# Kernel optimization log

Hardware: AMD Instinct MI355X
Metric: run time of the kernel (lower is better)

The kernel has to match this reference:

```python
import jax, jax.numpy as jnp
import numpy as np

B, SEQ, C_IN, F, K = 32, 16384, 64, 64, 9

def setup_inputs() -> dict:
    key = jax.random.key(0)
    k1, k2 = jax.random.split(key)
    x = jax.random.normal(k1, (B, SEQ, C_IN), dtype=jnp.float32)
    w = jax.random.normal(k2, (F, K, C_IN), dtype=jnp.float32) * 0.05  # mimics random_normal_initializer stddev
    b = jnp.zeros((F,), dtype=jnp.float32)
    return {"x": x, "w": w, "b": b}

def reference(x, w, b):
    # Faithful math: out[bt, t, f] = sum_{k,c} w[f,k,c] * x[bt, t+k, c] + b[f]
    # (VALID padding, stride 1). Expressed as an efficient conv instead of the
    # original unrolled loop + giant stacked intermediate.
    kernel = jnp.transpose(w, (1, 2, 0))  # [K, C_in, F] for WIO layout
    out = jax.lax.conv_general_dilated(
        x, kernel,
        window_strides=(1,),
        padding='VALID',
        dimension_numbers=('NWC', 'WIO', 'NWC'),
    )  # [B, SEQ-K+1, F]
    return out + b[None, None, :]
```

## Files before the change

### kernel.cpp

```cpp
#include <hip/hip_runtime.h>
#include <hip/hip_bf16.h>

#define T_IN   16384
#define T_OUT  16376
#define CIN    64
#define NF     64
#define KT     9
#define NB     32
#define TILE   128
#define ROWS   (TILE + KT - 1)
#define LDS_STRIDE 72
#define TILES_PER_BATCH 128
#define NTILES (NB * TILES_PER_BATCH)
#define NBLOCKS 512
#define TILE_ITERS (NTILES / NBLOCKS)

typedef __bf16 bf16x8 __attribute__((ext_vector_type(8)));
typedef unsigned short u16x8 __attribute__((ext_vector_type(8)));
typedef unsigned short u16x4 __attribute__((ext_vector_type(4)));
typedef float f32x16 __attribute__((ext_vector_type(16)));

__device__ __forceinline__ unsigned short f2bf(float f) {
    unsigned u = __builtin_bit_cast(unsigned, f);
    u += 0x7FFFu + ((u >> 16) & 1u);
    return (unsigned short)(u >> 16);
}

__global__ __launch_bounds__(256, 2) void conv1d_mfma_kernel(
    const float* __restrict__ x,
    const float* __restrict__ w,
    const float* __restrict__ b,
    float* __restrict__ out)
{
    __shared__ __attribute__((aligned(16))) unsigned short ldsX[ROWS * LDS_STRIDE];

    const int tid  = threadIdx.x;
    const int lane = tid & 63;
    const int wv   = tid >> 6;
    const int half = lane >> 5;
    const int l31  = lane & 31;
    const int fh   = wv & 1;
    const int rh   = wv >> 1;
    const int fbase = fh * 32;
    const int rbase = rh * 64;
    const int fcol  = fbase + l31;

    bf16x8 Bf[KT][4];
#pragma unroll
    for (int k = 0; k < KT; ++k) {
#pragma unroll
        for (int s = 0; s < 4; ++s) {
            const float* wp = w + (size_t)fcol * (KT * CIN) + k * CIN + s * 16 + half * 8;
            const float4 w0 = *(const float4*)(wp);
            const float4 w1 = *(const float4*)(wp + 4);
            u16x8 t;
            t[0] = f2bf(w0.x); t[1] = f2bf(w0.y); t[2] = f2bf(w0.z); t[3] = f2bf(w0.w);
            t[4] = f2bf(w1.x); t[5] = f2bf(w1.y); t[6] = f2bf(w1.z); t[7] = f2bf(w1.w);
            Bf[k][s] = __builtin_bit_cast(bf16x8, t);
        }
    }
    const float bias = b[fcol];

    for (int it = 0; it < TILE_ITERS; ++it) {
        const int g  = blockIdx.x * TILE_ITERS + it;
        const int bb = g >> 7;
        const int t0 = (g & 127) << 7;

        for (int i = tid; i < ROWS * 16; i += 256) {
            const int r  = i >> 4;
            const int cg = i & 15;
            int gr = t0 + r;
            gr = gr < (T_IN - 1) ? gr : (T_IN - 1);
            const float4 v = *(const float4*)(x + ((size_t)bb * T_IN + gr) * CIN + cg * 4);
            u16x4 p;
            p[0] = f2bf(v.x); p[1] = f2bf(v.y); p[2] = f2bf(v.z); p[3] = f2bf(v.w);
            *(u16x4*)&ldsX[r * LDS_STRIDE + cg * 4] = p;
        }
        __syncthreads();

        f32x16 acc0 = {0,0,0,0,0,0,0,0,0,0,0,0,0,0,0,0};
        f32x16 acc1 = {0,0,0,0,0,0,0,0,0,0,0,0,0,0,0,0};
        const int abase = (rbase + l31) * LDS_STRIDE + half * 8;
#pragma unroll
        for (int k = 0; k < KT; ++k) {
#pragma unroll
            for (int s = 0; s < 4; ++s) {
                const int off = abase + k * LDS_STRIDE + s * 16;
                bf16x8 a0 = *(const bf16x8*)&ldsX[off];
                bf16x8 a1 = *(const bf16x8*)&ldsX[off + 32 * LDS_STRIDE];
                acc0 = __builtin_amdgcn_mfma_f32_32x32x16_bf16(a0, Bf[k][s], acc0, 0, 0, 0);
                acc1 = __builtin_amdgcn_mfma_f32_32x32x16_bf16(a1, Bf[k][s], acc1, 0, 0, 0);
            }
        }

#pragma unroll
        for (int m = 0; m < 2; ++m) {
            const f32x16 A = m ? acc1 : acc0;
#pragma unroll
            for (int r = 0; r < 16; ++r) {
                const int tl = rbase + m * 32 + (r & 3) + 8 * (r >> 2) + 4 * half;
                const int tg = t0 + tl;
                if (tg < T_OUT)
                    out[((size_t)bb * T_OUT + tg) * NF + fcol] = A[r] + bias;
            }
        }
        __syncthreads();
    }
}

extern "C" void kernel_launch(void* const* d_in, const int* in_sizes, int n_in,
                              void* d_out, int out_size, void* d_ws, size_t ws_size,
                              hipStream_t stream) {
    const float* x = (const float*)d_in[0];
    const float* w = (const float*)d_in[1];
    const float* b = (const float*)d_in[2];
    float* out = (float*)d_out;
    conv1d_mfma_kernel<<<NBLOCKS, 256, 0, stream>>>(x, w, b, out);
}
```

Before: 295.0 us.

## Double-buffer LDS input tiles with register prefetch of next tile

Adds a second LDS buffer and prefetches the next tile's input into registers (9 float4 per thread) before the MFMA loop. After compute it converts the prefetched data to bf16, writes it to the other buffer, and synchronizes once per iteration instead of twice. The aim is to hide global load latency behind MFMA work. In exchange, register pressure rises by 36 VGPRs on top of the 144 already used for the weight fragments, which under launch_bounds(256,2) may cause spills. LDS use also doubles.

```diff
diff --git a/kernel.cpp b/kernel.cpp
--- a/kernel.cpp
+++ b/kernel.cpp
@@ -14,6 +14,8 @@
 #define NTILES (NB * TILES_PER_BATCH)
 #define NBLOCKS 512
 #define TILE_ITERS (NTILES / NBLOCKS)
+#define CHUNKS (ROWS * 16)
+#define CPT 9
 
 typedef __bf16 bf16x8 __attribute__((ext_vector_type(8)));
 typedef unsigned short u16x8 __attribute__((ext_vector_type(8)));
@@ -32,7 +34,7 @@
     const float* __restrict__ b,
     float* __restrict__ out)
 {
-    __shared__ __attribute__((aligned(16))) unsigned short ldsX[ROWS * LDS_STRIDE];
+    __shared__ __attribute__((aligned(16))) unsigned short ldsX[2][ROWS * LDS_STRIDE];
 
     const int tid  = threadIdx.x;
     const int lane = tid & 63;
@@ -61,36 +63,92 @@
     }
     const float bias = b[fcol];
 
-    for (int it = 0; it < TILE_ITERS; ++it) {
-        const int g  = blockIdx.x * TILE_ITERS + it;
+    float4 st[CPT];
+
+    {
+        const int g  = blockIdx.x * TILE_ITERS;
         const int bb = g >> 7;
         const int t0 = (g & 127) << 7;
+#pragma unroll
+        for (int i = 0; i < CPT; ++i) {
+            const int idx = i * 256 + tid;
+            if (idx < CHUNKS) {
+                const int r  = idx >> 4;
+                const int cg = idx & 15;
+                int gr = t0 + r;
+                gr = gr < (T_IN - 1) ? gr : (T_IN - 1);
+                st[i] = *(const float4*)(x + ((size_t)bb * T_IN + gr) * CIN + cg * 4);
+            }
+        }
+#pragma unroll
+        for (int i = 0; i < CPT; ++i) {
+            const int idx = i * 256 + tid;
+            if (idx < CHUNKS) {
+                const int r  = idx >> 4;
+                const int cg = idx & 15;
+                u16x4 p;
+                p[0] = f2bf(st[i].x); p[1] = f2bf(st[i].y);
+                p[2] = f2bf(st[i].z); p[3] = f2bf(st[i].w);
+                *(u16x4*)&ldsX[0][r * LDS_STRIDE + cg * 4] = p;
+            }
+        }
+    }
+    __syncthreads();
 
-        for (int i = tid; i < ROWS * 16; i += 256) {
-            const int r  = i >> 4;
-            const int cg = i & 15;
-            int gr = t0 + r;
-            gr = gr < (T_IN - 1) ? gr : (T_IN - 1);
-            const float4 v = *(const float4*)(x + ((size_t)bb * T_IN + gr) * CIN + cg * 4);
-            u16x4 p;
-            p[0] = f2bf(v.x); p[1] = f2bf(v.y); p[2] = f2bf(v.z); p[3] = f2bf(v.w);
-            *(u16x4*)&ldsX[r * LDS_STRIDE + cg * 4] = p;
+    for (int it = 0; it < TILE_ITERS; ++it) {
+        const int g   = blockIdx.x * TILE_ITERS + it;
+        const int bb  = g >> 7;
+        const int t0  = (g & 127) << 7;
+        const int cur = it & 1;
+        const bool more = (it + 1 < TILE_ITERS);
+
+        if (more) {
+            const int gn  = g + 1;
+            const int bbn = gn >> 7;
+            const int t0n = (gn & 127) << 7;
+#pragma unroll
+            for (int i = 0; i < CPT; ++i) {
+                const int idx = i * 256 + tid;
+                if (idx < CHUNKS) {
+                    const int r  = idx >> 4;
+                    const int cg = idx & 15;
+                    int gr = t0n + r;
+                    gr = gr < (T_IN - 1) ? gr : (T_IN - 1);
+                    st[i] = *(const float4*)(x + ((size_t)bbn * T_IN + gr) * CIN + cg * 4);
+                }
+            }
         }
-        __syncthreads();
 
         f32x16 acc0 = {0,0,0,0,0,0,0,0,0,0,0,0,0,0,0,0};
         f32x16 acc1 = {0,0,0,0,0,0,0,0,0,0,0,0,0,0,0,0};
+        const unsigned short* lx = ldsX[cur];
         const int abase = (rbase + l31) * LDS_STRIDE + half * 8;
 #pragma unroll
         for (int k = 0; k < KT; ++k) {
 #pragma unroll
             for (int s = 0; s < 4; ++s) {
                 const int off = abase + k * LDS_STRIDE + s * 16;
-                bf16x8 a0 = *(const bf16x8*)&ldsX[off];
-                bf16x8 a1 = *(const bf16x8*)&ldsX[off + 32 * LDS_STRIDE];
+                bf16x8 a0 = *(const bf16x8*)&lx[off];
+                bf16x8 a1 = *(const bf16x8*)&lx[off + 32 * LDS_STRIDE];
                 acc0 = __builtin_amdgcn_mfma_f32_32x32x16_bf16(a0, Bf[k][s], acc0, 0, 0, 0);
                 acc1 = __builtin_amdgcn_mfma_f32_32x32x16_bf16(a1, Bf[k][s], acc1, 0, 0, 0);
             }
+        }
+
+        if (more) {
+#pragma unroll
+            for (int i = 0; i < CPT; ++i) {
+                const int idx = i * 256 + tid;
+                if (idx < CHUNKS) {
+                    const int r  = idx >> 4;
+                    const int cg = idx & 15;
+                    u16x4 p;
+                    p[0] = f2bf(st[i].x); p[1] = f2bf(st[i].y);
+                    p[2] = f2bf(st[i].z); p[3] = f2bf(st[i].w);
+                    *(u16x4*)&ldsX[cur ^ 1][r * LDS_STRIDE + cg * 4] = p;
+                }
+            }
+            __syncthreads();
         }
 
 #pragma unroll
@@ -104,7 +162,6 @@
                     out[((size_t)bb * T_OUT + tg) * NF + fcol] = A[r] + bias;
             }
         }
-        __syncthreads();
     }
 }
 
```

After: 303.9 us. +3.0%, slower.

## Prefetch next input tile into LDS via async global_load_lds while computing

Applied to the files above, without the earlier changes.

Introduces an fp32 LDS staging buffer filled through global_load_lds DMA for the next tile while MFMAs run on the current one, then converts it to bf16 in LDS between barriers. This is meant to hide global-load latency behind compute. It adds about 35KB of LDS per block, which may limit occupancy below 2 blocks per CU, and it adds an extra LDS read-convert pass. The output stores now happen after the convert step.

```diff
diff --git a/kernel.cpp b/kernel.cpp
--- a/kernel.cpp
+++ b/kernel.cpp
@@ -14,6 +14,8 @@
 #define NTILES (NB * TILES_PER_BATCH)
 #define NBLOCKS 512
 #define TILE_ITERS (NTILES / NBLOCKS)
+#define CHUNKS (ROWS * 16)
+#define DMA_INSTR (ROWS / 4)
 
 typedef __bf16 bf16x8 __attribute__((ext_vector_type(8)));
 typedef unsigned short u16x8 __attribute__((ext_vector_type(8)));
@@ -26,12 +28,19 @@
     return (unsigned short)(u >> 16);
 }
 
+__device__ __forceinline__ void async_load16(const float* g, float* l) {
+    __builtin_amdgcn_global_load_lds(
+        (const __attribute__((address_space(1))) void*)g,
+        (__attribute__((address_space(3))) void*)l, 16, 0, 0);
+}
+
 __global__ __launch_bounds__(256, 2) void conv1d_mfma_kernel(
     const float* __restrict__ x,
     const float* __restrict__ w,
     const float* __restrict__ b,
     float* __restrict__ out)
 {
+    __shared__ __attribute__((aligned(16))) float          f32X[ROWS * CIN];
     __shared__ __attribute__((aligned(16))) unsigned short ldsX[ROWS * LDS_STRIDE];
 
     const int tid  = threadIdx.x;
@@ -44,6 +53,9 @@
     const int fbase = fh * 32;
     const int rbase = rh * 64;
     const int fcol  = fbase + l31;
+
+    const int dma_r = lane >> 4;
+    const int dma_c = (lane & 15) << 2;
 
     bf16x8 Bf[KT][4];
 #pragma unroll
@@ -61,22 +73,40 @@
     }
     const float bias = b[fcol];
 
-    for (int it = 0; it < TILE_ITERS; ++it) {
-        const int g  = blockIdx.x * TILE_ITERS + it;
+    auto stage = [&](int g) {
         const int bb = g >> 7;
         const int t0 = (g & 127) << 7;
+        for (int j = wv; j < DMA_INSTR; j += 4) {
+            int gr = t0 + j * 4 + dma_r;
+            gr = gr < (T_IN - 1) ? gr : (T_IN - 1);
+            const float* gp = x + ((size_t)bb * T_IN + gr) * CIN + dma_c;
+            async_load16(gp, &f32X[j * 256]);
+        }
+    };
 
-        for (int i = tid; i < ROWS * 16; i += 256) {
+    auto convert = [&]() {
+        for (int i = tid; i < CHUNKS; i += 256) {
+            const float4 v = *(const float4*)&f32X[i * 4];
             const int r  = i >> 4;
             const int cg = i & 15;
-            int gr = t0 + r;
-            gr = gr < (T_IN - 1) ? gr : (T_IN - 1);
-            const float4 v = *(const float4*)(x + ((size_t)bb * T_IN + gr) * CIN + cg * 4);
             u16x4 p;
             p[0] = f2bf(v.x); p[1] = f2bf(v.y); p[2] = f2bf(v.z); p[3] = f2bf(v.w);
             *(u16x4*)&ldsX[r * LDS_STRIDE + cg * 4] = p;
         }
-        __syncthreads();
+    };
+
+    stage(blockIdx.x * TILE_ITERS);
+    __syncthreads();
+    convert();
+    __syncthreads();
+
+    for (int it = 0; it < TILE_ITERS; ++it) {
+        const int g   = blockIdx.x * TILE_ITERS + it;
+        const int bb  = g >> 7;
+        const int t0  = (g & 127) << 7;
+        const bool more = (it + 1 < TILE_ITERS);
+
+        if (more) stage(g + 1);
 
         f32x16 acc0 = {0,0,0,0,0,0,0,0,0,0,0,0,0,0,0,0};
         f32x16 acc1 = {0,0,0,0,0,0,0,0,0,0,0,0,0,0,0,0};
@@ -93,6 +123,10 @@
             }
         }
 
+        __syncthreads();
+        if (more) convert();
+        __syncthreads();
+
 #pragma unroll
         for (int m = 0; m < 2; ++m) {
             const f32x16 A = m ? acc1 : acc0;
@@ -104,7 +138,6 @@
                     out[((size_t)bb * T_OUT + tg) * NF + fcol] = A[r] + bias;
             }
         }
-        __syncthreads();
     }
 }
 
```

Measured after the change: 291.1 us. Within noise of the previous version (-1.3%).

## Double-buffer LDS input tiles and prefetch two tiles ahead in registers

Applied to the files above, without the earlier changes.

Input staging becomes a software pipeline. The next tile's fp32 data is held in registers and converted into a second LDS buffer while the MFMA loop runs. Global loads for the tile two steps ahead are issued inside the k loop. This is meant to hide global load latency and drop one barrier per tile, in exchange for doubled LDS use and nine extra float4 registers per thread, which could reduce occupancy.

```diff
diff --git a/kernel.cpp b/kernel.cpp
--- a/kernel.cpp
+++ b/kernel.cpp
@@ -10,10 +10,9 @@
 #define TILE   128
 #define ROWS   (TILE + KT - 1)
 #define LDS_STRIDE 72
-#define TILES_PER_BATCH 128
-#define NTILES (NB * TILES_PER_BATCH)
 #define NBLOCKS 512
-#define TILE_ITERS (NTILES / NBLOCKS)
+#define TILE_ITERS 8
+#define CHUNKS (ROWS * 16)
 
 typedef __bf16 bf16x8 __attribute__((ext_vector_type(8)));
 typedef unsigned short u16x8 __attribute__((ext_vector_type(8)));
@@ -32,7 +31,7 @@
     const float* __restrict__ b,
     float* __restrict__ out)
 {
-    __shared__ __attribute__((aligned(16))) unsigned short ldsX[ROWS * LDS_STRIDE];
+    __shared__ __attribute__((aligned(16))) unsigned short ldsX[2][ROWS * LDS_STRIDE];
 
     const int tid  = threadIdx.x;
     const int lane = tid & 63;
@@ -41,9 +40,8 @@
     const int l31  = lane & 31;
     const int fh   = wv & 1;
     const int rh   = wv >> 1;
-    const int fbase = fh * 32;
     const int rbase = rh * 64;
-    const int fcol  = fbase + l31;
+    const int fcol  = fh * 32 + l31;
 
     bf16x8 Bf[KT][4];
 #pragma unroll
@@ -61,22 +59,48 @@
     }
     const float bias = b[fcol];
 
+    const int base = blockIdx.x * TILE_ITERS;
+
+    auto load_chunk = [&](int g, int k) -> float4 {
+        const int idx = k * 256 + tid;
+        const int r   = idx >> 4;
+        const int cg  = idx & 15;
+        const int bb2 = g >> 7;
+        int gr = ((g & 127) << 7) + r;
+        gr = gr < (T_IN - 1) ? gr : (T_IN - 1);
+        return *(const float4*)(x + ((size_t)bb2 * T_IN + gr) * CIN + cg * 4);
+    };
+
+    float4 st[KT];
+
+#pragma unroll
+    for (int k = 0; k < KT; ++k)
+        if (k < 8 || tid < 128) st[k] = load_chunk(base, k);
+#pragma unroll
+    for (int k = 0; k < KT; ++k) {
+        if (k < 8 || tid < 128) {
+            const int idx = k * 256 + tid;
+            const int r = idx >> 4, cg = idx & 15;
+            u16x4 p;
+            p[0] = f2bf(st[k].x); p[1] = f2bf(st[k].y);
+            p[2] = f2bf(st[k].z); p[3] = f2bf(st[k].w);
+            *(u16x4*)&ldsX[0][r * LDS_STRIDE + cg * 4] = p;
+        }
+    }
+#pragma unroll
+    for (int k = 0; k < KT; ++k)
+        if (k < 8 || tid < 128) st[k] = load_chunk(base + 1, k);
+    __syncthreads();
+
     for (int it = 0; it < TILE_ITERS; ++it) {
-        const int g  = blockIdx.x * TILE_ITERS + it;
+        const int g  = base + it;
         const int bb = g >> 7;
         const int t0 = (g & 127) << 7;
-
-        for (int i = tid; i < ROWS * 16; i += 256) {
-            const int r  = i >> 4;
-            const int cg = i & 15;
-            int gr = t0 + r;
-            gr = gr < (T_IN - 1) ? gr : (T_IN - 1);
-            const float4 v = *(const float4*)(x + ((size_t)bb * T_IN + gr) * CIN + cg * 4);
-            u16x4 p;
-            p[0] = f2bf(v.x); p[1] = f2bf(v.y); p[2] = f2bf(v.z); p[3] = f2bf(v.w);
-            *(u16x4*)&ldsX[r * LDS_STRIDE + cg * 4] = p;
-        }
-        __syncthreads();
+        const int c  = it & 1;
+        const unsigned short* lx = ldsX[c];
+        unsigned short*       lw = ldsX[c ^ 1];
+        const bool cons = (it < TILE_ITERS - 1);
+        const bool lood = (it < TILE_ITERS - 2);
 
         f32x16 acc0 = {0,0,0,0,0,0,0,0,0,0,0,0,0,0,0,0};
         f32x16 acc1 = {0,0,0,0,0,0,0,0,0,0,0,0,0,0,0,0};
@@ -86,10 +110,21 @@
 #pragma unroll
             for (int s = 0; s < 4; ++s) {
                 const int off = abase + k * LDS_STRIDE + s * 16;
-                bf16x8 a0 = *(const bf16x8*)&ldsX[off];
-                bf16x8 a1 = *(const bf16x8*)&ldsX[off + 32 * LDS_STRIDE];
+                bf16x8 a0 = *(const bf16x8*)&lx[off];
+                bf16x8 a1 = *(const bf16x8*)&lx[off + 32 * LDS_STRIDE];
                 acc0 = __builtin_amdgcn_mfma_f32_32x32x16_bf16(a0, Bf[k][s], acc0, 0, 0, 0);
                 acc1 = __builtin_amdgcn_mfma_f32_32x32x16_bf16(a1, Bf[k][s], acc1, 0, 0, 0);
+            }
+            if (cons && (k < 8 || tid < 128)) {
+                const int idx = k * 256 + tid;
+                const int r = idx >> 4, cg = idx & 15;
+                u16x4 p;
+                p[0] = f2bf(st[k].x); p[1] = f2bf(st[k].y);
+                p[2] = f2bf(st[k].z); p[3] = f2bf(st[k].w);
+                *(u16x4*)&lw[r * LDS_STRIDE + cg * 4] = p;
+            }
+            if (lood && (k < 8 || tid < 128)) {
+                st[k] = load_chunk(g + 2, k);
             }
         }
 
@@ -104,6 +139,7 @@
                     out[((size_t)bb * T_OUT + tg) * NF + fcol] = A[r] + bias;
             }
         }
+
         __syncthreads();
     }
 }
```

Result: slower. 302.5 us (+2.6%).
